# Kernel optimization log

Measured on AMD Instinct MI355X. Metric: run time of the kernel, lower is better.

## Reference

```python
import jax, jax.numpy as jnp
from jax import lax
import numpy as np

EPS = 1e-5
HEADS, DIM_K, R = 4, 16, 15
PAD = (R - 1) // 2


def bn(x, g, b, m, v):
    # inference-mode BatchNorm2d over channel dim 1
    scale = g * lax.rsqrt(v + EPS)
    return x * scale[None, :, None, None] + (b - m * scale)[None, :, None, None]


def conv1x1(x, w):
    # x: (B,Cin,H,W), w: (Cout,Cin)
    return jnp.einsum('bchw,oc->bohw', x, w)


def position_lambdas(emb, values):
    # emb: (K,R,R), values: (B,V,H,W) -> (B,K,V,H*W)
    # conv3d with kernel depth 1 == per-v-channel 2d conv with K output maps
    B, V, H, W = values.shape
    vals = values.reshape(B * V, 1, H, W)
    out = lax.conv_general_dilated(vals, emb[:, None, :, :], (1, 1),
                                   [(PAD, PAD), (PAD, PAD)])  # (B*V,K,H,W)
    out = out.reshape(B, V, DIM_K, H, W).transpose(0, 2, 1, 3, 4)
    return out.reshape(B, DIM_K, V, H * W)


def lambda_layer(x, q_w, bnq_g, bnq_b, bnq_m, bnq_v, k_w, v_w,
                 bnv_g, bnv_b, bnv_m, bnv_v, emb):
    B, _, H, W = x.shape
    q = bn(conv1x1(x, q_w), bnq_g, bnq_b, bnq_m, bnq_v)      # (B, K*heads, H, W)
    k = conv1x1(x, k_w)                                       # (B, K, H, W)
    v = bn(conv1x1(x, v_w), bnv_g, bnv_b, bnv_m, bnv_v)      # (B, V, H, W)
    pos = position_lambdas(emb, v)                            # (B, K, V, H*W)
    k = jax.nn.softmax(k, axis=1)                             # softmax over dim_k (as in source)
    dim_v = v.shape[1]
    q = q.reshape(B, HEADS, DIM_K, H * W)
    k = k.reshape(B, DIM_K, H * W)
    v2 = v.reshape(B, dim_v, H * W)
    content_lambda = jnp.einsum('bkm,bvm->bkv', k, v2)
    content_out = jnp.einsum('bhkn,bkv->bhvn', q, content_lambda)
    position_out = jnp.einsum('bhkn,bkvn->bhvn', q, pos)
    out = content_out + position_out                          # (B, heads, V, H*W)
    return out.reshape(B, HEADS * dim_v, H, W)


def setup_inputs() -> dict:
    key = jax.random.key(0)
    ks = jax.random.split(key, 32)
    inplanes, width, outplanes = 512, 128, 512
    dim_v = width // HEADS
    B, H, W = 32, 64, 64
    n = lambda i, shape, s=1.0: jax.random.normal(ks[i], shape, jnp.float32) * s
    u = lambda i, shape: jax.random.uniform(ks[i], shape, jnp.float32, 0.5, 1.5)
    return {
        'x': n(0, (B, inplanes, H, W)),
        'conv1_w': n(1, (width, inplanes), 0.05),
        'bn1_g': u(2, (width,)), 'bn1_b': n(3, (width,), 0.1),
        'bn1_m': n(4, (width,), 0.1), 'bn1_v': u(5, (width,)),
        'q_w': n(6, (DIM_K * HEADS, width), 0.05),
        'bnq_g': u(7, (DIM_K * HEADS,)), 'bnq_b': n(8, (DIM_K * HEADS,), 0.1),
        'bnq_m': n(9, (DIM_K * HEADS,), 0.1), 'bnq_v': u(10, (DIM_K * HEADS,)),
        'k_w': n(11, (DIM_K, width), 0.05),
        'v_w': n(12, (dim_v, width), 0.05),
        'bnv_g': u(13, (dim_v,)), 'bnv_b': n(14, (dim_v,), 0.1),
        'bnv_m': n(15, (dim_v,), 0.1), 'bnv_v': u(16, (dim_v,)),
        'emb': n(17, (DIM_K, R, R), 0.1),
        'bn2_g': u(18, (width,)), 'bn2_b': n(19, (width,), 0.1),
        'bn2_m': n(20, (width,), 0.1), 'bn2_v': u(21, (width,)),
        'conv3_w': n(22, (outplanes, width), 0.05),
        'bn3_g': u(23, (outplanes,)), 'bn3_b': n(24, (outplanes,), 0.1),
        'bn3_m': n(25, (outplanes,), 0.1), 'bn3_v': u(26, (outplanes,)),
    }


def reference(x, conv1_w, bn1_g, bn1_b, bn1_m, bn1_v,
              q_w, bnq_g, bnq_b, bnq_m, bnq_v, k_w, v_w,
              bnv_g, bnv_b, bnv_m, bnv_v, emb,
              bn2_g, bn2_b, bn2_m, bn2_v,
              conv3_w, bn3_g, bn3_b, bn3_m, bn3_v):
    residual = x
    h = jax.nn.relu(bn(conv1x1(x, conv1_w), bn1_g, bn1_b, bn1_m, bn1_v))
    h = lambda_layer(h, q_w, bnq_g, bnq_b, bnq_m, bnq_v, k_w, v_w,
                     bnv_g, bnv_b, bnv_m, bnv_v, emb)
    h = jax.nn.relu(bn(h, bn2_g, bn2_b, bn2_m, bn2_v))
    h = bn(conv1x1(h, conv3_w), bn3_g, bn3_b, bn3_m, bn3_v)
    return jax.nn.relu(h + residual)
```

## Files before the change

kernel.cpp:

```cpp
#include <hip/hip_runtime.h>

#define EPS 1e-5f

typedef __attribute__((ext_vector_type(8))) short bf16x8;
typedef __attribute__((ext_vector_type(8))) unsigned short u16x8;
typedef __attribute__((ext_vector_type(4))) float f32x4;

__device__ __forceinline__ unsigned short f2bf(float f) {
  union { float f; unsigned u; } c; c.f = f;
  unsigned u = c.u;
  u += 0x7FFFu + ((u >> 16) & 1u);
  return (unsigned short)(u >> 16);
}
__device__ __forceinline__ float bf2f(unsigned short h) {
  union { unsigned u; float f; } c; c.u = (unsigned)h << 16;
  return c.f;
}
__device__ __forceinline__ void gl_lds16(const void* gsrc, void* lds) {
  __builtin_amdgcn_global_load_lds(
      (const __attribute__((address_space(1))) unsigned*)gsrc,
      (__attribute__((address_space(3))) unsigned*)lds, 16, 0, 0);
}

__global__ __launch_bounds__(256) void k0_prep(
    const float* __restrict__ w1, const float* __restrict__ w3,
    unsigned short* __restrict__ w1bf, unsigned short* __restrict__ w3bf) {
  const int i = (blockIdx.x * 256 + threadIdx.x) * 4;
  const float* src = i < 65536 ? w1 + i : w3 + (i - 65536);
  unsigned short* dst = i < 65536 ? w1bf + i : w3bf + (i - 65536);
  float4 f = *reinterpret_cast<const float4*>(src);
  ushort4 o; o.x = f2bf(f.x); o.y = f2bf(f.y); o.z = f2bf(f.z); o.w = f2bf(f.w);
  *reinterpret_cast<ushort4*>(dst) = o;
}

__global__ __launch_bounds__(256) void k1_conv1(
    const float* __restrict__ x, const unsigned short* __restrict__ w1bf,
    const float* __restrict__ g1, const float* __restrict__ b1,
    const float* __restrict__ m1, const float* __restrict__ v1,
    unsigned short* __restrict__ h) {
  __shared__ unsigned short As[128 * 64];
  __shared__ unsigned short Bs[128 * 72];
  __shared__ float sc[128], bi[128];
  const int t = threadIdx.x;
  const int b = blockIdx.y;
  const int n0 = blockIdx.x * 128;
  if (t < 128) {
    float s = g1[t] * rsqrtf(v1[t] + EPS);
    sc[t] = s; bi[t] = b1[t] - m1[t] * s;
  }
  const int lane = t & 63, wv = t >> 6;
  const int wm = (wv >> 1) * 64, wn = (wv & 1) * 64;
  const int l15 = lane & 15, kg = lane >> 4;
  const int sl = lane & 7, rr = lane >> 3;
  f32x4 acc[4][4] = {};
  const float* xb = x + (size_t)b * 512 * 4096;
  const int cB = t >> 2, psB = (t & 3) * 8;
  for (int kt = 0; kt < 512; kt += 64) {
    __syncthreads();
    {
      const int r0 = wv * 32;
      #pragma unroll
      for (int j = 0; j < 4; j++) {
        const int row = r0 + j * 8 + rr;
        const int chunk = sl ^ (row & 7);
        gl_lds16(w1bf + row * 512 + kt + chunk * 8, &As[(r0 + j * 8) * 64]);
      }
    }
    {
      const float* src = xb + (size_t)(kt + cB) * 4096 + n0 + psB;
      #pragma unroll
      for (int j = 0; j < 4; j++) {
        float4 f0 = reinterpret_cast<const float4*>(src + 32 * j)[0];
        float4 f1 = reinterpret_cast<const float4*>(src + 32 * j)[1];
        float vals[8] = {f0.x, f0.y, f0.z, f0.w, f1.x, f1.y, f1.z, f1.w};
        #pragma unroll
        for (int e = 0; e < 8; e++) {
          const int px = psB + 32 * j + e;
          Bs[px * 72 + (((cB >> 3) ^ ((px >> 2) & 7)) << 3) + (cB & 7)] = f2bf(vals[e]);
        }
      }
    }
    __syncthreads();
    #pragma unroll
    for (int kk = 0; kk < 64; kk += 32) {
      const int c16 = kg + (kk >> 3);
      bf16x8 af[4], bf[4];
      #pragma unroll
      for (int mf = 0; mf < 4; mf++) {
        const int ch = wm + mf * 16 + l15;
        af[mf] = *reinterpret_cast<const bf16x8*>(&As[ch * 64 + ((c16 ^ (ch & 7)) << 3)]);
      }
      #pragma unroll
      for (int nf = 0; nf < 4; nf++) {
        const int px = wn + nf * 16 + l15;
        bf[nf] = *reinterpret_cast<const bf16x8*>(
            &Bs[px * 72 + ((c16 ^ ((px >> 2) & 7)) << 3)]);
      }
      #pragma unroll
      for (int mf = 0; mf < 4; mf++)
        #pragma unroll
        for (int nf = 0; nf < 4; nf++)
          acc[mf][nf] = __builtin_amdgcn_mfma_f32_16x16x32_bf16(
              af[mf], bf[nf], acc[mf][nf], 0, 0, 0);
    }
  }
  unsigned short* hb = h + (size_t)b * 128 * 4096;
  #pragma unroll
  for (int mf = 0; mf < 4; mf++)
    #pragma unroll
    for (int nf = 0; nf < 4; nf++) {
      const int px = n0 + wn + nf * 16 + l15;
      #pragma unroll
      for (int r = 0; r < 4; r++) {
        const int ch = wm + mf * 16 + 4 * kg + r;
        float val = fmaxf(fmaf(acc[mf][nf][r], sc[ch], bi[ch]), 0.f);
        hb[(size_t)ch * 4096 + px] = f2bf(val);
      }
    }
}

__global__ __launch_bounds__(256) void k2_qkv(
    const unsigned short* __restrict__ h,
    const float* __restrict__ qw, const float* __restrict__ kw,
    const float* __restrict__ vw,
    const float* __restrict__ gq, const float* __restrict__ bq,
    const float* __restrict__ mq, const float* __restrict__ vq,
    const float* __restrict__ gv, const float* __restrict__ bv,
    const float* __restrict__ mv, const float* __restrict__ vv,
    unsigned short* __restrict__ qo, unsigned short* __restrict__ ko,
    unsigned short* __restrict__ vo) {
  __shared__ unsigned short As[112 * 72];
  __shared__ unsigned short Bs[64 * 72];
  __shared__ float sc[112], bi[112];
  const int t = threadIdx.x, b = blockIdx.y, n0 = blockIdx.x * 64;
  if (t < 112) {
    float s, bb;
    if (t < 64)      { s = gq[t] * rsqrtf(vq[t] + EPS); bb = bq[t] - mq[t] * s; }
    else if (t < 80) { s = 1.f; bb = 0.f; }
    else { int c = t - 80; s = gv[c] * rsqrtf(vv[c] + EPS); bb = bv[c] - mv[c] * s; }
    sc[t] = s; bi[t] = bb;
  }
  const int lane = t & 63, wv = t >> 6;
  const int l15 = lane & 15, kg = lane >> 4;
  f32x4 acc[7] = {};
  const unsigned short* hb = h + (size_t)b * 128 * 4096;
  for (int kt = 0; kt < 128; kt += 64) {
    __syncthreads();
    for (int e = t; e < 112 * 64; e += 256) {
      const int row = e >> 6, kk2 = e & 63, gk = kt + kk2;
      float val = row < 64 ? qw[row * 128 + gk]
                : row < 80 ? kw[(row - 64) * 128 + gk]
                           : vw[(row - 80) * 128 + gk];
      As[row * 72 + kk2] = f2bf(val);
    }
    {
      const int c = t >> 2, p0 = (t & 3) * 16;
      const unsigned short* src = hb + (size_t)(kt + c) * 4096 + n0 + p0;
      #pragma unroll
      for (int i = 0; i < 4; i++) {
        ushort4 u = reinterpret_cast<const ushort4*>(src)[i];
        const int p = p0 + 4 * i;
        Bs[(p + 0) * 72 + c] = u.x; Bs[(p + 1) * 72 + c] = u.y;
        Bs[(p + 2) * 72 + c] = u.z; Bs[(p + 3) * 72 + c] = u.w;
      }
    }
    __syncthreads();
    #pragma unroll
    for (int kk = 0; kk < 64; kk += 32) {
      bf16x8 bfr = *reinterpret_cast<const bf16x8*>(
          &Bs[(wv * 16 + l15) * 72 + kk + 8 * kg]);
      #pragma unroll
      for (int mf = 0; mf < 7; mf++) {
        bf16x8 af = *reinterpret_cast<const bf16x8*>(
            &As[(mf * 16 + l15) * 72 + kk + 8 * kg]);
        acc[mf] = __builtin_amdgcn_mfma_f32_16x16x32_bf16(af, bfr, acc[mf], 0, 0, 0);
      }
    }
  }
  const int px = n0 + wv * 16 + l15;
  float e0[4];
  float mx = -1e30f;
  #pragma unroll
  for (int r = 0; r < 4; r++) mx = fmaxf(mx, acc[4][r]);
  mx = fmaxf(mx, __shfl_xor(mx, 16));
  mx = fmaxf(mx, __shfl_xor(mx, 32));
  float s = 0.f;
  #pragma unroll
  for (int r = 0; r < 4; r++) { e0[r] = expf(acc[4][r] - mx); s += e0[r]; }
  s += __shfl_xor(s, 16); s += __shfl_xor(s, 32);
  const float inv = 1.f / s;
  #pragma unroll
  for (int mf = 0; mf < 7; mf++) {
    #pragma unroll
    for (int r = 0; r < 4; r++) {
      const int row = mf * 16 + 4 * kg + r;
      if (mf == 4) {
        ko[((size_t)b * 16 + (row - 64)) * 4096 + px] = f2bf(e0[r] * inv);
      } else {
        float val = fmaf(acc[mf][r], sc[row], bi[row]);
        if (row < 64) qo[((size_t)b * 64 + row) * 4096 + px] = f2bf(val);
        else          vo[((size_t)b * 32 + (row - 80)) * 4096 + px] = f2bf(val);
      }
    }
  }
}

__global__ __launch_bounds__(256) void k3_lambda(
    const unsigned short* __restrict__ ko, const unsigned short* __restrict__ vo,
    float* __restrict__ lc) {
  const int t = threadIdx.x, b = blockIdx.x;
  const int kc = t >> 4, pl = t & 15;
  const unsigned short* kb = ko + ((size_t)b * 16 + kc) * 4096;
  const unsigned short* vb = vo + (size_t)b * 32 * 4096;
  float acc[32] = {};
  for (int i = 0; i < 256; i++) {
    const int pix = pl + 16 * i;
    const float kv = bf2f(kb[pix]);
    #pragma unroll
    for (int vc = 0; vc < 32; vc++)
      acc[vc] = fmaf(kv, bf2f(vb[vc * 4096 + pix]), acc[vc]);
  }
  #pragma unroll
  for (int vc = 0; vc < 32; vc++) {
    float a = acc[vc];
    a += __shfl_xor(a, 1); a += __shfl_xor(a, 2);
    a += __shfl_xor(a, 4); a += __shfl_xor(a, 8);
    acc[vc] = a;
  }
  if (pl == 0) {
    #pragma unroll
    for (int vc = 0; vc < 32; vc++)
      lc[((size_t)b * 16 + kc) * 32 + vc] = acc[vc];
  }
}

__global__ __launch_bounds__(256) void k4_pos(
    const unsigned short* __restrict__ qo, const unsigned short* __restrict__ vo,
    const float* __restrict__ lc, const float* __restrict__ emb,
    const float* __restrict__ g2, const float* __restrict__ b2,
    const float* __restrict__ m2, const float* __restrict__ v2,
    unsigned short* __restrict__ g) {
  __shared__ unsigned short vh[30784];
  __shared__ float lcs[512];
  __shared__ float sc[128], bi[128];
  const int t = threadIdx.x, b = blockIdx.y, tile = blockIdx.x;
  const int ty = (tile >> 2) * 16, tx = (tile & 3) * 16;
  const int lane = t & 63, wv = t >> 6;
  const int px = lane & 15, kg = lane >> 4;
  if (t < 128) { float s = g2[t] * rsqrtf(v2[t] + EPS); sc[t] = s; bi[t] = b2[t] - m2[t] * s; }
  for (int e = t; e < 512; e += 256) lcs[e] = lc[b * 512 + e];
  {
    unsigned* vz = reinterpret_cast<unsigned*>(vh);
    for (int i = t; i < 15392; i += 256) vz[i] = 0;
  }
  bf16x8 ef[8];
  #pragma unroll
  for (int c = 0; c < 8; c++) {
    #pragma unroll
    for (int j = 0; j < 8; j++) {
      const int kd = 32 * c + 8 * kg + j;
      const int dy = kd >> 4, dx = kd & 15;
      float val = (dy < 15 && dx < 15) ? emb[(px * 15 + dy) * 15 + dx] : 0.f;
      ef[c][j] = (short)f2bf(val);
    }
  }
  __syncthreads();
  const unsigned short* vb = vo + (size_t)b * 32 * 4096;
  for (int r = t; r < 960; r += 256) {
    const int vc = r / 30, yy = r % 30;
    const int gy = ty + yy - 7;
    if (gy >= 0 && gy < 64) {
      const int x0 = tx - 7;
      const int xs = x0 < 0 ? -x0 : 0;
      const int xe = (x0 + 30 > 64) ? (64 - x0) : 30;
      const unsigned short* src = vb + vc * 4096 + gy * 64 + x0;
      unsigned short* dst = vh + (vc * 30 + yy) * 32;
      for (int xx = xs; xx < xe; xx++) dst[xx] = src[xx];
    }
  }
  __syncthreads();
  const unsigned short* qb = qo + (size_t)b * 64 * 4096;
  unsigned short* gb = g + (size_t)b * 128 * 4096;
  const int dyk = kg >> 1, dx0 = (kg & 1) * 8;
  for (int nbi = 0; nbi < 4; nbi++) {
    const int nb = wv * 4 + nbi;
    const int pixg = (ty + nb) * 64 + tx + px;
    float qr[4][4];
    #pragma unroll
    for (int hh = 0; hh < 4; hh++)
      #pragma unroll
      for (int r = 0; r < 4; r++)
        qr[hh][r] = bf2f(qb[(size_t)(hh * 16 + 4 * kg + r) * 4096 + pixg]);
    auto emit = [&](const f32x4& a, int vc2) {
      float s0 = 0, s1 = 0, s2 = 0, s3 = 0;
      #pragma unroll
      for (int r = 0; r < 4; r++) {
        const float p = a[r] + lcs[(4 * kg + r) * 32 + vc2];
        s0 = fmaf(qr[0][r], p, s0); s1 = fmaf(qr[1][r], p, s1);
        s2 = fmaf(qr[2][r], p, s2); s3 = fmaf(qr[3][r], p, s3);
      }
      s0 += __shfl_xor(s0, 16); s0 += __shfl_xor(s0, 32);
      s1 += __shfl_xor(s1, 16); s1 += __shfl_xor(s1, 32);
      s2 += __shfl_xor(s2, 16); s2 += __shfl_xor(s2, 32);
      s3 += __shfl_xor(s3, 16); s3 += __shfl_xor(s3, 32);
      const float ssel = kg == 0 ? s0 : kg == 1 ? s1 : kg == 2 ? s2 : s3;
      const int ch = kg * 32 + vc2;
      float val = fmaxf(fmaf(ssel, sc[ch], bi[ch]), 0.f);
      gb[(size_t)ch * 4096 + pixg] = f2bf(val);
    };
    for (int vc = 0; vc < 32; vc += 2) {
      f32x4 a0 = {}, a1 = {};
      #pragma unroll
      for (int c = 0; c < 8; c++) {
        const int yy = nb + 2 * c + dyk;
        const unsigned short* p0 = &vh[(vc * 30 + yy) * 32 + px + dx0];
        const unsigned short* p1 = p0 + 960;
        bf16x8 b0, b1;
        #pragma unroll
        for (int j = 0; j < 8; j++) { b0[j] = (short)p0[j]; b1[j] = (short)p1[j]; }
        a0 = __builtin_amdgcn_mfma_f32_16x16x32_bf16(ef[c], b0, a0, 0, 0, 0);
        a1 = __builtin_amdgcn_mfma_f32_16x16x32_bf16(ef[c], b1, a1, 0, 0, 0);
      }
      emit(a0, vc);
      emit(a1, vc + 1);
    }
  }
}

__global__ __launch_bounds__(256) void k5_conv3(
    const unsigned short* __restrict__ g, const unsigned short* __restrict__ w3bf,
    const float* __restrict__ g3, const float* __restrict__ b3,
    const float* __restrict__ m3, const float* __restrict__ v3,
    const float* __restrict__ x, float* __restrict__ out) {
  __shared__ unsigned short As[128 * 72];
  __shared__ unsigned short Bs[128 * 64];
  __shared__ float sc[128], bi[128];
  const int t = threadIdx.x;
  const int n0 = blockIdx.x * 128, m0 = blockIdx.y * 128, b = blockIdx.z;
  if (t < 128) {
    const int ch = m0 + t;
    float s = g3[ch] * rsqrtf(v3[ch] + EPS);
    sc[t] = s; bi[t] = b3[ch] - m3[ch] * s;
  }
  const int lane = t & 63, wv = t >> 6;
  const int wpx = (wv >> 1) * 64, wch = (wv & 1) * 64;
  const int l15 = lane & 15, kg = lane >> 4;
  const int sl = lane & 7, rr = lane >> 3;
  f32x4 acc[4][4] = {};
  const unsigned short* gb = g + (size_t)b * 128 * 4096;
  const int cA = t >> 2, psA = (t & 3) * 8;
  for (int kt = 0; kt < 128; kt += 64) {
    __syncthreads();
    {
      const unsigned short* src = gb + (size_t)(kt + cA) * 4096 + n0 + psA;
      #pragma unroll
      for (int j = 0; j < 4; j++) {
        u16x8 u = *reinterpret_cast<const u16x8*>(src + 32 * j);
        #pragma unroll
        for (int e = 0; e < 8; e++) {
          const int px = psA + 32 * j + e;
          As[px * 72 + (((cA >> 3) ^ ((px >> 2) & 7)) << 3) + (cA & 7)] = u[e];
        }
      }
    }
    {
      const int r0 = wv * 32;
      #pragma unroll
      for (int j = 0; j < 4; j++) {
        const int row = r0 + j * 8 + rr;
        const int chunk = sl ^ (row & 7);
        gl_lds16(w3bf + (size_t)(m0 + row) * 128 + kt + chunk * 8,
                 &Bs[(r0 + j * 8) * 64]);
      }
    }
    __syncthreads();
    #pragma unroll
    for (int kk = 0; kk < 64; kk += 32) {
      const int c16 = kg + (kk >> 3);
      bf16x8 af[4], bf[4];
      #pragma unroll
      for (int mf = 0; mf < 4; mf++) {
        const int px = wpx + mf * 16 + l15;
        af[mf] = *reinterpret_cast<const bf16x8*>(
            &As[px * 72 + ((c16 ^ ((px >> 2) & 7)) << 3)]);
      }
      #pragma unroll
      for (int nf = 0; nf < 4; nf++) {
        const int row = wch + nf * 16 + l15;
        bf[nf] = *reinterpret_cast<const bf16x8*>(
            &Bs[row * 64 + ((c16 ^ (row & 7)) << 3)]);
      }
      #pragma unroll
      for (int mf = 0; mf < 4; mf++)
        #pragma unroll
        for (int nf = 0; nf < 4; nf++)
          acc[mf][nf] = __builtin_amdgcn_mfma_f32_16x16x32_bf16(
              af[mf], bf[nf], acc[mf][nf], 0, 0, 0);
    }
  }
  #pragma unroll
  for (int mf = 0; mf < 4; mf++)
    #pragma unroll
    for (int nf = 0; nf < 4; nf++) {
      const int chl = wch + nf * 16 + l15;
      const size_t base = ((size_t)b * 512 + m0 + chl) * 4096 +
                          (n0 + wpx + mf * 16 + 4 * kg);
      float4 xv = *reinterpret_cast<const float4*>(x + base);
      float4 o;
      o.x = fmaxf(fmaf(acc[mf][nf][0], sc[chl], bi[chl]) + xv.x, 0.f);
      o.y = fmaxf(fmaf(acc[mf][nf][1], sc[chl], bi[chl]) + xv.y, 0.f);
      o.z = fmaxf(fmaf(acc[mf][nf][2], sc[chl], bi[chl]) + xv.z, 0.f);
      o.w = fmaxf(fmaf(acc[mf][nf][3], sc[chl], bi[chl]) + xv.w, 0.f);
      *reinterpret_cast<float4*>(out + base) = o;
    }
}

extern "C" void kernel_launch(void* const* d_in, const int* in_sizes, int n_in,
                              void* d_out, int out_size, void* d_ws, size_t ws_size,
                              hipStream_t stream) {
  (void)in_sizes; (void)n_in; (void)out_size; (void)ws_size;
  const float* x   = (const float*)d_in[0];
  const float* w1  = (const float*)d_in[1];
  const float* g1  = (const float*)d_in[2];
  const float* b1  = (const float*)d_in[3];
  const float* m1  = (const float*)d_in[4];
  const float* v1  = (const float*)d_in[5];
  const float* qw  = (const float*)d_in[6];
  const float* gq  = (const float*)d_in[7];
  const float* bq  = (const float*)d_in[8];
  const float* mq  = (const float*)d_in[9];
  const float* vq  = (const float*)d_in[10];
  const float* kw  = (const float*)d_in[11];
  const float* vw  = (const float*)d_in[12];
  const float* gv  = (const float*)d_in[13];
  const float* bv  = (const float*)d_in[14];
  const float* mv  = (const float*)d_in[15];
  const float* vv  = (const float*)d_in[16];
  const float* emb = (const float*)d_in[17];
  const float* g2  = (const float*)d_in[18];
  const float* b2  = (const float*)d_in[19];
  const float* m2  = (const float*)d_in[20];
  const float* v2  = (const float*)d_in[21];
  const float* w3  = (const float*)d_in[22];
  const float* g3  = (const float*)d_in[23];
  const float* b3  = (const float*)d_in[24];
  const float* m3  = (const float*)d_in[25];
  const float* v3  = (const float*)d_in[26];
  float* out = (float*)d_out;

  char* ws = (char*)d_ws;
  unsigned short* hbuf = (unsigned short*)(ws);
  unsigned short* qbuf = (unsigned short*)(ws + 33554432);
  unsigned short* kbuf = (unsigned short*)(ws + 50331648);
  unsigned short* vbuf = (unsigned short*)(ws + 54525952);
  float*          lcb  = (float*)        (ws + 62914560);
  unsigned short* w1bf = (unsigned short*)(ws + 62980096);
  unsigned short* w3bf = (unsigned short*)(ws + 63111168);

  k0_prep<<<dim3(128), 256, 0, stream>>>(w1, w3, w1bf, w3bf);
  k1_conv1<<<dim3(32, 32), 256, 0, stream>>>(x, w1bf, g1, b1, m1, v1, hbuf);
  k2_qkv<<<dim3(64, 32), 256, 0, stream>>>(hbuf, qw, kw, vw, gq, bq, mq, vq,
                                           gv, bv, mv, vv, qbuf, kbuf, vbuf);
  k3_lambda<<<dim3(32), 256, 0, stream>>>(kbuf, vbuf, lcb);
  k4_pos<<<dim3(16, 32), 256, 0, stream>>>(qbuf, vbuf, lcb, emb, g2, b2, m2, v2, hbuf);
  k5_conv3<<<dim3(32, 4, 32), 256, 0, stream>>>(hbuf, w3bf, g3, b3, m3, v3, x, out);
}
```

Measured before the change: 1.041 ms.

## Restructure position-conv LDS layout and use transposed LDS reads for MFMA operands

Rewrites the k4_pos position-lambda kernel. The halo tile is now staged in LDS as two 16-column planes per value channel, loaded with 16-byte vector copies instead of scalar ones, and the MFMA B operands are gathered with ds_read_b64_tr_b16 transposed reads in place of per-element ushort loads. The embedding A fragments are re-mapped to match the new layout. The cross-lane head reduction is reorganised so each lane does three shuffles instead of six, and the content lambda is pre-transposed for float4 loads. The goal is to cut LDS instruction count and shuffle overhead. It relies on gfx950-specific inline asm and careful offset arithmetic.

```diff
diff --git a/kernel.cpp b/kernel.cpp
--- a/kernel.cpp
+++ b/kernel.cpp
@@ -5,6 +5,8 @@
 typedef __attribute__((ext_vector_type(8))) short bf16x8;
 typedef __attribute__((ext_vector_type(8))) unsigned short u16x8;
 typedef __attribute__((ext_vector_type(4))) float f32x4;
+typedef __attribute__((ext_vector_type(2))) unsigned u32x2;
+typedef __attribute__((ext_vector_type(4))) unsigned u32x4;
 
 __device__ __forceinline__ unsigned short f2bf(float f) {
   union { float f; unsigned u; } c; c.f = f;
@@ -20,6 +22,11 @@
   __builtin_amdgcn_global_load_lds(
       (const __attribute__((address_space(1))) unsigned*)gsrc,
       (__attribute__((address_space(3))) unsigned*)lds, 16, 0, 0);
+}
+__device__ __forceinline__ float sel4(int i, float a, float b, float c, float d) {
+  float lo = (i & 1) ? b : a;
+  float hi = (i & 1) ? d : c;
+  return (i & 2) ? hi : lo;
 }
 
 __global__ __launch_bounds__(256) void k0_prep(
@@ -240,91 +247,119 @@
     const float* __restrict__ g2, const float* __restrict__ b2,
     const float* __restrict__ m2, const float* __restrict__ v2,
     unsigned short* __restrict__ g) {
-  __shared__ unsigned short vh[30784];
-  __shared__ float lcs[512];
+  __shared__ unsigned short vh[32 * 2 * 32 * 16];
+  __shared__ float lcs2[512];
   __shared__ float sc[128], bi[128];
   const int t = threadIdx.x, b = blockIdx.y, tile = blockIdx.x;
   const int ty = (tile >> 2) * 16, tx = (tile & 3) * 16;
   const int lane = t & 63, wv = t >> 6;
   const int px = lane & 15, kg = lane >> 4;
   if (t < 128) { float s = g2[t] * rsqrtf(v2[t] + EPS); sc[t] = s; bi[t] = b2[t] - m2[t] * s; }
-  for (int e = t; e < 512; e += 256) lcs[e] = lc[b * 512 + e];
+  for (int e = t; e < 512; e += 256) {
+    const int vc = e >> 4, kch = e & 15;
+    lcs2[e] = lc[b * 512 + kch * 32 + vc];
+  }
   {
-    unsigned* vz = reinterpret_cast<unsigned*>(vh);
-    for (int i = t; i < 15392; i += 256) vz[i] = 0;
-  }
-  bf16x8 ef[8];
-  #pragma unroll
-  for (int c = 0; c < 8; c++) {
+    u32x4 z = {0, 0, 0, 0};
+    for (int i = t; i < 4096; i += 256)
+      *reinterpret_cast<u32x4*>(&vh[i * 8]) = z;
+  }
+  bf16x8 af[8];
+  #pragma unroll
+  for (int m = 0; m < 8; m++) {
     #pragma unroll
     for (int j = 0; j < 8; j++) {
-      const int kd = 32 * c + 8 * kg + j;
-      const int dy = kd >> 4, dx = kd & 15;
+      const int dy = 4 * (m & 3) + (j & 3);
+      const int dx = kg + 4 * (j >> 2) + 8 * (m >> 2);
       float val = (dy < 15 && dx < 15) ? emb[(px * 15 + dy) * 15 + dx] : 0.f;
-      ef[c][j] = (short)f2bf(val);
+      af[m][j] = (short)f2bf(val);
     }
   }
   __syncthreads();
   const unsigned short* vb = vo + (size_t)b * 32 * 4096;
-  for (int r = t; r < 960; r += 256) {
-    const int vc = r / 30, yy = r % 30;
-    const int gy = ty + yy - 7;
-    if (gy >= 0 && gy < 64) {
-      const int x0 = tx - 7;
-      const int xs = x0 < 0 ? -x0 : 0;
-      const int xe = (x0 + 30 > 64) ? (64 - x0) : 30;
-      const unsigned short* src = vb + vc * 4096 + gy * 64 + x0;
-      unsigned short* dst = vh + (vc * 30 + yy) * 32;
-      for (int xx = xs; xx < xe; xx++) dst[xx] = src[xx];
+  for (int task = t; task < 32 * 2 * 30 * 2; task += 256) {
+    const int half = task & 1, row = (task >> 1) % 30, pv = (task >> 1) / 30;
+    const int p = pv & 1, vc = pv >> 1;
+    const int gy = ty + row - 7;
+    const int gx = tx - 8 + p * 16 + half * 8;
+    if (gy >= 0 && gy < 64 && gx >= 0 && gx <= 56) {
+      u16x8 u = *reinterpret_cast<const u16x8*>(vb + vc * 4096 + gy * 64 + gx);
+      *reinterpret_cast<u16x8*>(&vh[((vc * 2 + p) * 32 + row) * 16 + half * 8]) = u;
     }
   }
   __syncthreads();
+
+  unsigned fo[4];
+  #pragma unroll
+  for (int c = 0; c < 4; c++) {
+    const int col = px + kg + 1 + 4 * c;
+    fo[c] = (unsigned)((col >> 4) * 1024 + (col & 15) * 2);
+  }
+  const unsigned vhOFF = (unsigned)(size_t)(&vh[0]);
   const unsigned short* qb = qo + (size_t)b * 64 * 4096;
   unsigned short* gb = g + (size_t)b * 128 * 4096;
-  const int dyk = kg >> 1, dx0 = (kg & 1) * 8;
-  for (int nbi = 0; nbi < 4; nbi++) {
-    const int nb = wv * 4 + nbi;
-    const int pixg = (ty + nb) * 64 + tx + px;
+
+#define TRRD(dst, areg, IMM) \
+  asm volatile("ds_read_b64_tr_b16 %0, %1 offset:" IMM : "=v"(dst) : "v"(areg))
+
+  for (int yi = 0; yi < 4; yi++) {
+    const int ylocal = wv * 4 + yi;
+    const int pixg = (ty + ylocal) * 64 + tx + px;
     float qr[4][4];
     #pragma unroll
     for (int hh = 0; hh < 4; hh++)
       #pragma unroll
       for (int r = 0; r < 4; r++)
         qr[hh][r] = bf2f(qb[(size_t)(hh * 16 + 4 * kg + r) * 4096 + pixg]);
-    auto emit = [&](const f32x4& a, int vc2) {
-      float s0 = 0, s1 = 0, s2 = 0, s3 = 0;
-      #pragma unroll
-      for (int r = 0; r < 4; r++) {
-        const float p = a[r] + lcs[(4 * kg + r) * 32 + vc2];
-        s0 = fmaf(qr[0][r], p, s0); s1 = fmaf(qr[1][r], p, s1);
-        s2 = fmaf(qr[2][r], p, s2); s3 = fmaf(qr[3][r], p, s3);
-      }
-      s0 += __shfl_xor(s0, 16); s0 += __shfl_xor(s0, 32);
-      s1 += __shfl_xor(s1, 16); s1 += __shfl_xor(s1, 32);
-      s2 += __shfl_xor(s2, 16); s2 += __shfl_xor(s2, 32);
-      s3 += __shfl_xor(s3, 16); s3 += __shfl_xor(s3, 32);
-      const float ssel = kg == 0 ? s0 : kg == 1 ? s1 : kg == 2 ? s2 : s3;
-      const int ch = kg * 32 + vc2;
-      float val = fmaxf(fmaf(ssel, sc[ch], bi[ch]), 0.f);
+    const unsigned rowb = vhOFF + (unsigned)(ylocal * 32);
+    for (int vc = 0; vc < 32; vc++) {
+      const unsigned vb0 = rowb + (unsigned)(vc * 2048);
+      const unsigned a0 = vb0 + fo[0], a1 = vb0 + fo[1];
+      const unsigned a2 = vb0 + fo[2], a3 = vb0 + fo[3];
+      u32x2 tr0[8], tr1[8];
+      TRRD(tr0[0], a0, "0");   TRRD(tr1[0], a1, "0");
+      TRRD(tr0[1], a0, "128"); TRRD(tr1[1], a1, "128");
+      TRRD(tr0[2], a0, "256"); TRRD(tr1[2], a1, "256");
+      TRRD(tr0[3], a0, "384"); TRRD(tr1[3], a1, "384");
+      TRRD(tr0[4], a2, "0");   TRRD(tr1[4], a3, "0");
+      TRRD(tr0[5], a2, "128"); TRRD(tr1[5], a3, "128");
+      TRRD(tr0[6], a2, "256"); TRRD(tr1[6], a3, "256");
+      TRRD(tr0[7], a2, "384"); TRRD(tr1[7], a3, "384");
+      float4 lcv = *reinterpret_cast<const float4*>(&lcs2[vc * 16 + kg * 4]);
+      asm volatile("s_waitcnt lgkmcnt(0)" ::: "memory");
+      __builtin_amdgcn_sched_barrier(0);
+      f32x4 acc = {0.f, 0.f, 0.f, 0.f};
+      #pragma unroll
+      for (int m = 0; m < 8; m++) {
+        u32x4 u;
+        u[0] = tr0[m][0]; u[1] = tr0[m][1];
+        u[2] = tr1[m][0]; u[3] = tr1[m][1];
+        acc = __builtin_amdgcn_mfma_f32_16x16x32_bf16(
+            af[m], __builtin_bit_cast(bf16x8, u), acc, 0, 0, 0);
+      }
+      float p0 = acc[0] + lcv.x, p1 = acc[1] + lcv.y;
+      float p2 = acc[2] + lcv.z, p3 = acc[3] + lcv.w;
+      float s0 = qr[0][0] * p0; s0 = fmaf(qr[0][1], p1, s0);
+      s0 = fmaf(qr[0][2], p2, s0); s0 = fmaf(qr[0][3], p3, s0);
+      float s1 = qr[1][0] * p0; s1 = fmaf(qr[1][1], p1, s1);
+      s1 = fmaf(qr[1][2], p2, s1); s1 = fmaf(qr[1][3], p3, s1);
+      float s2 = qr[2][0] * p0; s2 = fmaf(qr[2][1], p1, s2);
+      s2 = fmaf(qr[2][2], p2, s2); s2 = fmaf(qr[2][3], p3, s2);
+      float s3 = qr[3][0] * p0; s3 = fmaf(qr[3][1], p1, s3);
+      s3 = fmaf(qr[3][2], p2, s3); s3 = fmaf(qr[3][3], p3, s3);
+      float skg = sel4(kg,     s0, s1, s2, s3);
+      float sx1 = sel4(kg ^ 1, s0, s1, s2, s3);
+      float sx2 = sel4(kg ^ 2, s0, s1, s2, s3);
+      float sx3 = sel4(kg ^ 3, s0, s1, s2, s3);
+      float tt  = skg + __shfl_xor(sx1, 16);
+      float tt2 = sx2 + __shfl_xor(sx3, 16);
+      float S   = tt + __shfl_xor(tt2, 32);
+      const int ch = kg * 32 + vc;
+      float val = fmaxf(fmaf(S, sc[ch], bi[ch]), 0.f);
       gb[(size_t)ch * 4096 + pixg] = f2bf(val);
-    };
-    for (int vc = 0; vc < 32; vc += 2) {
-      f32x4 a0 = {}, a1 = {};
-      #pragma unroll
-      for (int c = 0; c < 8; c++) {
-        const int yy = nb + 2 * c + dyk;
-        const unsigned short* p0 = &vh[(vc * 30 + yy) * 32 + px + dx0];
-        const unsigned short* p1 = p0 + 960;
-        bf16x8 b0, b1;
-        #pragma unroll
-        for (int j = 0; j < 8; j++) { b0[j] = (short)p0[j]; b1[j] = (short)p1[j]; }
-        a0 = __builtin_amdgcn_mfma_f32_16x16x32_bf16(ef[c], b0, a0, 0, 0, 0);
-        a1 = __builtin_amdgcn_mfma_f32_16x16x32_bf16(ef[c], b1, a1, 0, 0, 0);
-      }
-      emit(a0, vc);
-      emit(a1, vc + 1);
-    }
-  }
+    }
+  }
+#undef TRRD
 }
 
 __global__ __launch_bounds__(256) void k5_conv3(
```

After: 834.9 us. 1.25x faster.
